# Kernel optimization log

Measured on AMD Instinct MI355X. Metric: run time of the kernel, lower is better.

Reference implementation:

```python
import jax, jax.numpy as jnp
import numpy as np

N = 50000      # nodes
E = 800000     # edges (before self-loops)
H = 4          # heads
C = 32         # hidden per head (hidden*heads = 128); out_channels = 32
IN = 128
NEG_SLOPE = 0.2


def setup_inputs() -> dict:
    key = jax.random.key(0)
    ks = jax.random.split(key, 16)
    s = 0.1
    d = {
        "x": jax.random.normal(ks[0], (N, IN), jnp.float32),
        "edge_index": jax.random.randint(ks[1], (2, E), 0, N),
        "edge_type": jax.random.randint(ks[2], (E,), 0, 38),
        "node_type": jax.random.randint(ks[3], (N,), 0, 4),
        # layer 1: in=128 -> H*C, concat
        "W1": jax.random.normal(ks[4], (IN, H * C), jnp.float32) * s,
        "a1s": jax.random.normal(ks[5], (H, C), jnp.float32) * s,
        "a1d": jax.random.normal(ks[6], (H, C), jnp.float32) * s,
        "b1": jnp.zeros((H * C,), jnp.float32),
        # layer 2: H*C -> H*C, concat
        "W2": jax.random.normal(ks[7], (H * C, H * C), jnp.float32) * s,
        "a2s": jax.random.normal(ks[8], (H, C), jnp.float32) * s,
        "a2d": jax.random.normal(ks[9], (H, C), jnp.float32) * s,
        "b2": jnp.zeros((H * C,), jnp.float32),
        # layer 3: H*C -> C, heads=1, mean (concat=False)
        "W3": jax.random.normal(ks[10], (H * C, C), jnp.float32) * s,
        "a3s": jax.random.normal(ks[11], (1, C), jnp.float32) * s,
        "a3d": jax.random.normal(ks[12], (1, C), jnp.float32) * s,
        "b3": jnp.zeros((C,), jnp.float32),
    }
    return d


def gat_layer(x, src, dst, W, a_s, a_d, b, heads, concat):
    # PyG GATConv (eval mode): linear, per-edge attention logits, segment
    # softmax over incoming edges at dst, weighted scatter-sum, bias.
    h = (x @ W).reshape(N, heads, -1)            # [N, H, C]
    al_s = jnp.einsum('nhc,hc->nh', h, a_s)       # [N, H]
    al_d = jnp.einsum('nhc,hc->nh', h, a_d)
    e = jax.nn.leaky_relu(al_s[src] + al_d[dst], NEG_SLOPE)   # [E', H]
    m = jax.ops.segment_max(e, dst, num_segments=N)            # [N, H]
    p = jnp.exp(e - m[dst])
    z = jax.ops.segment_sum(p, dst, num_segments=N)            # [N, H]
    alpha = p / (z[dst] + 1e-16)                               # [E', H]
    out = jax.ops.segment_sum(h[src] * alpha[..., None], dst, num_segments=N)  # [N, H, C]
    out = out.reshape(N, -1) if concat else out.mean(axis=1)
    return out + b


def reference(x, edge_index, edge_type, node_type,
              W1, a1s, a1d, b1, W2, a2s, a2d, b2, W3, a3s, a3d, b3):
    # add self-loops (PyG GATConv default add_self_loops=True)
    loop = jnp.arange(N, dtype=edge_index.dtype)
    src = jnp.concatenate([edge_index[0], loop])
    dst = jnp.concatenate([edge_index[1], loop])
    h = gat_layer(x, src, dst, W1, a1s, a1d, b1, H, True)
    h = jax.nn.elu(h)
    h = gat_layer(h, src, dst, W2, a2s, a2d, b2, H, True)
    h = jax.nn.elu(h)
    out = gat_layer(h, src, dst, W3, a3s, a3d, b3, 1, False)
    return out
```

## Files before the change

### kernel.cpp

```cpp
#include <hip/hip_runtime.h>
#include <hip/hip_fp16.h>

#define LRELU_SLOPE 0.2f
#define BSH 8
#define EPB 3584

typedef _Float16 f16x8 __attribute__((ext_vector_type(8)));
typedef float f32x4 __attribute__((ext_vector_type(4)));

__device__ __forceinline__ float lrelu(float x) { return x >= 0.0f ? x : LRELU_SLOPE * x; }

__device__ __forceinline__ float sel4(float a, float b, float c, float d, int h) {
  float r = a;
  r = (h == 1) ? b : r;
  r = (h == 2) ? c : r;
  r = (h == 3) ? d : r;
  return r;
}


__device__ __forceinline__ void prep_one(const float* __restrict__ W, __half* __restrict__ out,
                                         int NT, int t) {
  int l = t & 63, f = t >> 6;
  int kt = f / NT, nt = f % NT;
  int k0 = kt * 32 + (l >> 4) * 8;
  int col = nt * 16 + (l & 15);
  union { __half h[8]; float4 v; } u;
#pragma unroll
  for (int j = 0; j < 8; ++j) u.h[j] = (__half)W[(size_t)(k0 + j) * (NT * 16) + col];
  *(float4*)(out + (size_t)t * 8) = u.v;
}


__global__ void k_zero(int* __restrict__ bcnt) { bcnt[threadIdx.x] = 0; }

__global__ __launch_bounds__(256) void k_bcnt(
    const int* __restrict__ dst, int E, int* __restrict__ bcnt, int cntBlocks,
    const float* __restrict__ W1, __half* __restrict__ wf1,
    const float* __restrict__ W2, __half* __restrict__ wf2,
    const float* __restrict__ W3, __half* __restrict__ wf3) {
  if (blockIdx.x >= cntBlocks) {
    int t = (blockIdx.x - cntBlocks) * 256 + threadIdx.x;
    if (t < 2048) prep_one(W1, wf1, 8, t);
    else if (t < 4096) prep_one(W2, wf2, 8, t - 2048);
    else if (t < 4608) prep_one(W3, wf3, 2, t - 4096);
    return;
  }
  __shared__ int c[256];
  int t = threadIdx.x;
  c[t] = 0;
  __syncthreads();
  int e = (blockIdx.x * 256 + t) * 4;
  if (e + 3 < E) {
    int4 d = *(const int4*)&dst[e];
    atomicAdd(&c[d.x >> BSH], 1);
    atomicAdd(&c[d.y >> BSH], 1);
    atomicAdd(&c[d.z >> BSH], 1);
    atomicAdd(&c[d.w >> BSH], 1);
  } else {
    for (; e < E; ++e) atomicAdd(&c[dst[e] >> BSH], 1);
  }
  __syncthreads();
  if (c[t] > 0) atomicAdd(&bcnt[t], c[t]);
}

__global__ __launch_bounds__(256) void k_bscan(const int* __restrict__ bcnt,
                                               int* __restrict__ gcur,
                                               int* __restrict__ bbase, int E) {
  __shared__ int sm[256];
  int t = threadIdx.x;
  int v = bcnt[t];
  sm[t] = v;
  __syncthreads();
#pragma unroll
  for (int off = 1; off < 256; off <<= 1) {
    int u = (t >= off) ? sm[t - off] : 0;
    __syncthreads();
    sm[t] += u;
    __syncthreads();
  }
  int ex = sm[t] - v;
  gcur[t] = ex;
  bbase[t] = ex;
  if (t == 255) bbase[256] = E;
}


__device__ __forceinline__ f16x8 load_a(const float* xp) {
  float4 lo = *(const float4*)xp;
  float4 hi = *(const float4*)(xp + 4);
  f16x8 a;
  a[0] = (_Float16)lo.x; a[1] = (_Float16)lo.y; a[2] = (_Float16)lo.z; a[3] = (_Float16)lo.w;
  a[4] = (_Float16)hi.x; a[5] = (_Float16)hi.y; a[6] = (_Float16)hi.z; a[7] = (_Float16)hi.w;
  return a;
}

__device__ __forceinline__ f16x8 load_a(const __half* xp) {
  return *(const f16x8*)xp;
}

template <int NT, int NH, typename IN, typename OUT>
__device__ __forceinline__ void gemm_body(
    const IN* __restrict__ x, const __half* __restrict__ wfrag,
    const float* __restrict__ a_s, const float* __restrict__ a_d,
    OUT* __restrict__ h, float* __restrict__ als, float* __restrict__ ald,
    int n, int ntiles, int tile, int lane) {
  const f16x8* wf = (const f16x8*)wfrag;
  f16x8 B[4][NT];
#pragma unroll
  for (int kt = 0; kt < 4; ++kt)
#pragma unroll
    for (int nt = 0; nt < NT; ++nt) B[kt][nt] = wf[(kt * NT + nt) * 64 + lane];
  if (tile >= ntiles) return;
  int r0 = tile * 16;
  int arow = r0 + (lane & 15);
  const IN* xp = x + (size_t)arow * 128 + (lane >> 4) * 8;
  bool full = (r0 + 16 <= n);
  f16x8 A[4];
#pragma unroll
  for (int kt = 0; kt < 4; ++kt) {
    if (full || arow < n) A[kt] = load_a(xp + kt * 32);
    else A[kt] = (f16x8){};
  }
  f32x4 acc[NT];
#pragma unroll
  for (int nt = 0; nt < NT; ++nt) acc[nt] = (f32x4){0.f, 0.f, 0.f, 0.f};
#pragma unroll
  for (int kt = 0; kt < 4; ++kt)
#pragma unroll
    for (int nt = 0; nt < NT; ++nt)
      acc[nt] = __builtin_amdgcn_mfma_f32_16x16x32_f16(A[kt], B[kt][nt], acc[nt], 0, 0, 0);
  int cb = lane & 15, rb = (lane >> 4) * 4;
  float asv[NT], adv[NT];
#pragma unroll
  for (int nt = 0; nt < NT; ++nt) {
    asv[nt] = a_s[nt * 16 + cb];
    adv[nt] = a_d[nt * 16 + cb];
  }
#pragma unroll
  for (int r = 0; r < 4; ++r) {
    int row = r0 + rb + r;
    if (!full && row >= n) break;
#pragma unroll
    for (int nt = 0; nt < NT; ++nt)
      h[(size_t)row * (NT * 16) + nt * 16 + cb] = (OUT)acc[nt][r];
    if (NH == 4) {
      float ps[4], pd[4];
#pragma unroll
      for (int hh = 0; hh < 4; ++hh) {
        ps[hh] = acc[2 * hh][r] * asv[2 * hh] + acc[2 * hh + 1][r] * asv[2 * hh + 1];
        pd[hh] = acc[2 * hh][r] * adv[2 * hh] + acc[2 * hh + 1][r] * adv[2 * hh + 1];
      }
#pragma unroll
      for (int off = 1; off < 16; off <<= 1) {
#pragma unroll
        for (int hh = 0; hh < 4; ++hh) {
          ps[hh] += __shfl_xor(ps[hh], off);
          pd[hh] += __shfl_xor(pd[hh], off);
        }
      }
      if (cb < 4) {
        als[row * 4 + cb] = sel4(ps[0], ps[1], ps[2], ps[3], cb);
        ald[row * 4 + cb] = sel4(pd[0], pd[1], pd[2], pd[3], cb);
      }
    } else {
      float ps = acc[0][r] * asv[0] + acc[1][r] * asv[1];
      float pd = acc[0][r] * adv[0] + acc[1][r] * adv[1];
#pragma unroll
      for (int off = 1; off < 16; off <<= 1) {
        ps += __shfl_xor(ps, off);
        pd += __shfl_xor(pd, off);
      }
      if (cb == 0) { als[row] = ps; ald[row] = pd; }
    }
  }
}

template <int NT, int NH, typename IN, typename OUT>
__global__ __launch_bounds__(256, 2) void gemm_mfma(
    const IN* __restrict__ x, const __half* __restrict__ wfrag,
    const float* __restrict__ a_s, const float* __restrict__ a_d,
    OUT* __restrict__ h, float* __restrict__ als, float* __restrict__ ald,
    int n, int ntiles) {
  int lane = threadIdx.x & 63, w = threadIdx.x >> 6;
  gemm_body<NT, NH, IN, OUT>(x, wfrag, a_s, a_d, h, als, ald, n, ntiles,
                             blockIdx.x * 4 + w, lane);
}


__global__ __launch_bounds__(256) void k_bucket_gemm(
    const int* __restrict__ ei, int E, int* __restrict__ gcur, int2* __restrict__ ebuck,
    int bblocks,
    const float* __restrict__ x, const __half* __restrict__ wf1,
    const float* __restrict__ a1s, const float* __restrict__ a1d,
    __half* __restrict__ hA, float* __restrict__ als, float* __restrict__ ald,
    int n, int ntiles) {
  __shared__ int2 stage[EPB];
  __shared__ int cnt[256], offs[256], gbase[256], curl[256], sm[256];
  if (blockIdx.x >= bblocks) {
    int lane = threadIdx.x & 63, w = threadIdx.x >> 6;
    gemm_body<8, 4, float, __half>(x, wf1, a1s, a1d, hA, als, ald, n, ntiles,
                                   (blockIdx.x - bblocks) * 4 + w, lane);
    return;
  }
  int t = threadIdx.x;
  int base = blockIdx.x * EPB;
  int count = E - base;
  if (count > EPB) count = EPB;
  if (count < 0) count = 0;
  cnt[t] = 0;
  __syncthreads();
  for (int i = t; i < count; i += 256) {
    int d = ei[E + base + i];
    atomicAdd(&cnt[d >> BSH], 1);
  }
  __syncthreads();
  sm[t] = cnt[t];
  __syncthreads();
#pragma unroll
  for (int off = 1; off < 256; off <<= 1) {
    int u = (t >= off) ? sm[t - off] : 0;
    __syncthreads();
    sm[t] += u;
    __syncthreads();
  }
  offs[t] = sm[t] - cnt[t];
  curl[t] = sm[t] - cnt[t];
  if (cnt[t] > 0) gbase[t] = atomicAdd(&gcur[t], cnt[t]);
  __syncthreads();
  for (int i = t; i < count; i += 256) {
    int s = ei[base + i];
    int d = ei[E + base + i];
    int r = atomicAdd(&curl[d >> BSH], 1);
    stage[r] = make_int2(s, d);
  }
  __syncthreads();
  for (int i = t; i < count; i += 256) {
    int2 e = stage[i];
    int b = e.y >> BSH;
    ebuck[gbase[b] + (i - offs[b])] = e;
  }
}

__global__ __launch_bounds__(256) void k_fine(const int2* __restrict__ ebuck,
                                              const int* __restrict__ bbase,
                                              int* __restrict__ rowptr,
                                              int* __restrict__ colx, int n, int E) {
  __shared__ int cnt[256], cur[256], sm[256];
  int b = blockIdx.x, t = threadIdx.x;
  int lo = b << BSH;
  int hi = lo + 256;
  if (hi > n) hi = n;
  int nn = hi - lo;
  int ebeg = bbase[b], eend = bbase[b + 1];
  cnt[t] = 0;
  __syncthreads();
  for (int i = ebeg + t; i < eend; i += 256)
    atomicAdd(&cnt[ebuck[i].y - lo], 1);
  __syncthreads();
  sm[t] = cnt[t];
  __syncthreads();
#pragma unroll
  for (int off = 1; off < 256; off <<= 1) {
    int u = (t >= off) ? sm[t - off] : 0;
    __syncthreads();
    sm[t] += u;
    __syncthreads();
  }
  int nodebase = ebeg + sm[t] - cnt[t];
  if (t < nn) {
    rowptr[lo + t] = nodebase;
    cur[t] = nodebase;
  }
  if (t == 0 && b == gridDim.x - 1) rowptr[n] = E;
  __syncthreads();
  for (int i = ebeg + t; i < eend; i += 256) {
    int2 e = ebuck[i];
    int p = atomicAdd(&cur[e.y - lo], 1);
    colx[p] = e.x;
  }
}


__global__ __launch_bounds__(256) void k_agg128(
    const __half* __restrict__ h, const float* __restrict__ als,
    const float* __restrict__ ald, const int* __restrict__ rowptr,
    const int* __restrict__ colx, const float* __restrict__ bias,
    __half* __restrict__ out, int n) {
  int w = threadIdx.x >> 6, lane = threadIdx.x & 63;
  int node = blockIdx.x * 4 + w;
  if (node >= n) return;
  int g = lane >> 4, q = lane & 15, head = q >> 2;
  int beg = rowptr[node], end = rowptr[node + 1];
  float adh = ald[node * 4 + head];
  float acc[8] = {};
  float z = 0.f;
  if (g == 0) {
    float ws = __expf(lrelu(als[node * 4 + head] + adh));
    z = ws;
    float4 raw = *(const float4*)(h + (size_t)node * 128 + q * 8);
    const __half2* hh = (const __half2*)&raw;
#pragma unroll
    for (int j = 0; j < 4; ++j) {
      float2 f = __half22float2(hh[j]);
      acc[2 * j] = ws * f.x;
      acc[2 * j + 1] = ws * f.y;
    }
  }
  for (int e = beg + g; e < end; e += 4) {
    int s = colx[e];
    float wv = __expf(lrelu(als[s * 4 + head] + adh));
    float4 raw = *(const float4*)(h + (size_t)s * 128 + q * 8);
    const __half2* hh = (const __half2*)&raw;
    z += wv;
#pragma unroll
    for (int j = 0; j < 4; ++j) {
      float2 f = __half22float2(hh[j]);
      acc[2 * j] = fmaf(wv, f.x, acc[2 * j]);
      acc[2 * j + 1] = fmaf(wv, f.y, acc[2 * j + 1]);
    }
  }
#pragma unroll
  for (int off = 16; off <= 32; off <<= 1) {
    z += __shfl_xor(z, off);
#pragma unroll
    for (int j = 0; j < 8; ++j) acc[j] += __shfl_xor(acc[j], off);
  }
  if (g == 0) {
    float inv = 1.f / z;
    int c0 = q * 8;
    union { __half h8[8]; float4 v; } u;
#pragma unroll
    for (int j = 0; j < 8; ++j) {
      float v = acc[j] * inv + bias[c0 + j];
      v = (v > 0.f) ? v : (__expf(v) - 1.f);
      u.h8[j] = (__half)v;
    }
    *(float4*)&out[(size_t)node * 128 + c0] = u.v;
  }
}


__global__ __launch_bounds__(256) void k_agg32(
    const __half* __restrict__ h, const float* __restrict__ als,
    const float* __restrict__ ald, const int* __restrict__ rowptr,
    const int* __restrict__ colx, const float* __restrict__ bias,
    float* __restrict__ out, int n) {
  int w = threadIdx.x >> 6, lane = threadIdx.x & 63;
  int node = blockIdx.x * 4 + w;
  if (node >= n) return;
  int g = lane >> 4, q = lane & 15;
  int beg = rowptr[node], end = rowptr[node + 1];
  float ad = ald[node];
  float acc0 = 0.f, acc1 = 0.f, z = 0.f;
  if (g == 0) {
    float ws = __expf(lrelu(als[node] + ad));
    float2 f = __half22float2(*(const __half2*)&h[(size_t)node * 32 + 2 * q]);
    z = ws;
    acc0 = ws * f.x;
    acc1 = ws * f.y;
  }
  for (int e = beg + g; e < end; e += 4) {
    int s = colx[e];
    float wv = __expf(lrelu(als[s] + ad));
    float2 f = __half22float2(*(const __half2*)&h[(size_t)s * 32 + 2 * q]);
    z += wv;
    acc0 = fmaf(wv, f.x, acc0);
    acc1 = fmaf(wv, f.y, acc1);
  }
#pragma unroll
  for (int off = 16; off <= 32; off <<= 1) {
    z += __shfl_xor(z, off);
    acc0 += __shfl_xor(acc0, off);
    acc1 += __shfl_xor(acc1, off);
  }
  if (g == 0) {
    float inv = 1.f / z;
    *(float2*)&out[(size_t)node * 32 + 2 * q] =
        make_float2(acc0 * inv + bias[2 * q], acc1 * inv + bias[2 * q + 1]);
  }
}


extern "C" void kernel_launch(void* const* d_in, const int* in_sizes, int n_in,
                              void* d_out, int out_size, void* d_ws, size_t ws_size,
                              hipStream_t stream) {
  const float* x   = (const float*)d_in[0];
  const int*   ei  = (const int*)d_in[1];
  const float* W1  = (const float*)d_in[4];
  const float* a1s = (const float*)d_in[5];
  const float* a1d = (const float*)d_in[6];
  const float* b1  = (const float*)d_in[7];
  const float* W2  = (const float*)d_in[8];
  const float* a2s = (const float*)d_in[9];
  const float* a2d = (const float*)d_in[10];
  const float* b2  = (const float*)d_in[11];
  const float* W3  = (const float*)d_in[12];
  const float* a3s = (const float*)d_in[13];
  const float* a3d = (const float*)d_in[14];
  const float* b3  = (const float*)d_in[15];
  const int N = in_sizes[0] / 128;
  const int E = in_sizes[1] / 2;
  const int ntiles = (N + 15) / 16;
  const int nbuck = (N + 255) >> BSH;

  char* ws = (char*)d_ws;
  size_t off = 0;
  auto alloc = [&](size_t bytes) -> void* {
    void* p = ws + off;
    off += (bytes + 255) & ~(size_t)255;
    return p;
  };
  __half* hA    = (__half*)alloc((size_t)N * 128 * 2);
  __half* hB    = (__half*)alloc((size_t)N * 128 * 2);
  __half* h32   = (__half*)alloc((size_t)N * 32 * 2);
  float*  als_a = (float*)alloc((size_t)N * 4 * 4);
  float*  ald_a = (float*)alloc((size_t)N * 4 * 4);
  float*  als_b = (float*)alloc((size_t)N * 4 * 4);
  float*  ald_b = (float*)alloc((size_t)N * 4 * 4);
  float*  als1  = (float*)alloc((size_t)N * 4);
  float*  ald1  = (float*)alloc((size_t)N * 4);
  int* rowptr   = (int*)alloc((size_t)(N + 1) * 4);
  int* bcnt     = (int*)alloc(256 * 4);
  int* gcur     = (int*)alloc(256 * 4);
  int* bbase    = (int*)alloc(257 * 4);
  int2* ebuck   = (int2*)alloc((size_t)E * 8);
  int* colx     = (int*)alloc((size_t)E * 4);
  __half* wf1   = (__half*)alloc(4 * 8 * 64 * 8 * 2);
  __half* wf2   = (__half*)alloc(4 * 8 * 64 * 8 * 2);
  __half* wf3   = (__half*)alloc(4 * 2 * 64 * 8 * 2);
  (void)ws_size; (void)n_in; (void)out_size;

  k_zero<<<1, 256, 0, stream>>>(bcnt);
  int cntBlocks = (E / 4 + 255) / 256;
  k_bcnt<<<cntBlocks + 18, 256, 0, stream>>>(ei + E, E, bcnt, cntBlocks,
                                             W1, wf1, W2, wf2, W3, wf3);
  k_bscan<<<1, 256, 0, stream>>>(bcnt, gcur, bbase, E);

  int gblk = (ntiles + 3) / 4;
  int bblocks = (E + EPB - 1) / EPB;
  k_bucket_gemm<<<bblocks + gblk, 256, 0, stream>>>(ei, E, gcur, ebuck, bblocks,
                                                    x, wf1, a1s, a1d, hA, als_a, ald_a,
                                                    N, ntiles);
  k_fine<<<nbuck, 256, 0, stream>>>(ebuck, bbase, rowptr, colx, N, E);

  k_agg128<<<(N + 3) / 4, 256, 0, stream>>>(hA, als_a, ald_a, rowptr, colx, b1, hB, N);
  gemm_mfma<8, 4, __half, __half><<<gblk, 256, 0, stream>>>(hB, wf2, a2s, a2d, hA,
                                                            als_b, ald_b, N, ntiles);
  k_agg128<<<(N + 3) / 4, 256, 0, stream>>>(hA, als_b, ald_b, rowptr, colx, b2, hB, N);
  gemm_mfma<2, 1, __half, __half><<<gblk, 256, 0, stream>>>(hB, wf3, a3s, a3d, h32,
                                                            als1, ald1, N, ntiles);
  k_agg32<<<(N + 3) / 4, 256, 0, stream>>>(h32, als1, ald1, rowptr, colx, b3,
                                           (float*)d_out, N);
}
```

Baseline: 190.0 us.

## Pack bucketed edges into 32-bit words, drop zero kernel, widen aggregation lanes

Bucket counting now writes per-block partial histograms that the scan kernel sums, which removes the zero-init launch and the global atomics. Bucketed edges are packed as (src<<8 | dst&255) in 32 bits, with bucket ids staged separately in shared memory, halving the ebuck traffic. The aggregation kernels now use 8 edge groups of 8 lanes, each lane handling 16 (or 4) channels, which doubles edge-level parallelism and makes per-lane loads wider but adds an extra shuffle-reduction step and more registers per lane. Packing assumes source indices fit in 24 bits.

```diff
diff --git a/kernel.cpp b/kernel.cpp
--- a/kernel.cpp
+++ b/kernel.cpp
@@ -4,6 +4,7 @@
 #define LRELU_SLOPE 0.2f
 #define BSH 8
 #define EPB 3584
+#define EPC 8192
 
 typedef _Float16 f16x8 __attribute__((ext_vector_type(8)));
 typedef float f32x4 __attribute__((ext_vector_type(4)));
@@ -32,10 +33,8 @@
 }
 
 
-__global__ void k_zero(int* __restrict__ bcnt) { bcnt[threadIdx.x] = 0; }
-
 __global__ __launch_bounds__(256) void k_bcnt(
-    const int* __restrict__ dst, int E, int* __restrict__ bcnt, int cntBlocks,
+    const int* __restrict__ dst, int E, int* __restrict__ part, int cntBlocks,
     const float* __restrict__ W1, __half* __restrict__ wf1,
     const float* __restrict__ W2, __half* __restrict__ wf2,
     const float* __restrict__ W3, __half* __restrict__ wf3) {
@@ -50,26 +49,31 @@
   int t = threadIdx.x;
   c[t] = 0;
   __syncthreads();
-  int e = (blockIdx.x * 256 + t) * 4;
-  if (e + 3 < E) {
-    int4 d = *(const int4*)&dst[e];
-    atomicAdd(&c[d.x >> BSH], 1);
-    atomicAdd(&c[d.y >> BSH], 1);
-    atomicAdd(&c[d.z >> BSH], 1);
-    atomicAdd(&c[d.w >> BSH], 1);
-  } else {
-    for (; e < E; ++e) atomicAdd(&c[dst[e] >> BSH], 1);
-  }
-  __syncthreads();
-  if (c[t] > 0) atomicAdd(&bcnt[t], c[t]);
-}
-
-__global__ __launch_bounds__(256) void k_bscan(const int* __restrict__ bcnt,
+  int base = blockIdx.x * EPC;
+#pragma unroll
+  for (int k = 0; k < 8; ++k) {
+    int e = base + (k * 256 + t) * 4;
+    if (e + 3 < E) {
+      int4 d = *(const int4*)&dst[e];
+      atomicAdd(&c[d.x >> BSH], 1);
+      atomicAdd(&c[d.y >> BSH], 1);
+      atomicAdd(&c[d.z >> BSH], 1);
+      atomicAdd(&c[d.w >> BSH], 1);
+    } else {
+      for (int j = e; j < E && j < e + 4; ++j) atomicAdd(&c[dst[j] >> BSH], 1);
+    }
+  }
+  __syncthreads();
+  part[blockIdx.x * 256 + t] = c[t];
+}
+
+__global__ __launch_bounds__(256) void k_bscan(const int* __restrict__ part, int nb,
                                                int* __restrict__ gcur,
                                                int* __restrict__ bbase, int E) {
   __shared__ int sm[256];
   int t = threadIdx.x;
-  int v = bcnt[t];
+  int v = 0;
+  for (int b = 0; b < nb; ++b) v += part[b * 256 + t];
   sm[t] = v;
   __syncthreads();
 #pragma unroll
@@ -189,13 +193,14 @@
 
 
 __global__ __launch_bounds__(256) void k_bucket_gemm(
-    const int* __restrict__ ei, int E, int* __restrict__ gcur, int2* __restrict__ ebuck,
+    const int* __restrict__ ei, int E, int* __restrict__ gcur, int* __restrict__ ebuck,
     int bblocks,
     const float* __restrict__ x, const __half* __restrict__ wf1,
     const float* __restrict__ a1s, const float* __restrict__ a1d,
     __half* __restrict__ hA, float* __restrict__ als, float* __restrict__ ald,
     int n, int ntiles) {
-  __shared__ int2 stage[EPB];
+  __shared__ int stage[EPB];
+  __shared__ unsigned char bucket8[EPB];
   __shared__ int cnt[256], offs[256], gbase[256], curl[256], sm[256];
   if (blockIdx.x >= bblocks) {
     int lane = threadIdx.x & 63, w = threadIdx.x >> 6;
@@ -231,18 +236,19 @@
   for (int i = t; i < count; i += 256) {
     int s = ei[base + i];
     int d = ei[E + base + i];
-    int r = atomicAdd(&curl[d >> BSH], 1);
-    stage[r] = make_int2(s, d);
+    int b = d >> BSH;
+    int r = atomicAdd(&curl[b], 1);
+    stage[r] = (s << 8) | (d & 255);
+    bucket8[r] = (unsigned char)b;
   }
   __syncthreads();
   for (int i = t; i < count; i += 256) {
-    int2 e = stage[i];
-    int b = e.y >> BSH;
-    ebuck[gbase[b] + (i - offs[b])] = e;
-  }
-}
-
-__global__ __launch_bounds__(256) void k_fine(const int2* __restrict__ ebuck,
+    int b = bucket8[i];
+    ebuck[gbase[b] + (i - offs[b])] = stage[i];
+  }
+}
+
+__global__ __launch_bounds__(256) void k_fine(const int* __restrict__ ebuck,
                                               const int* __restrict__ bbase,
                                               int* __restrict__ rowptr,
                                               int* __restrict__ colx, int n, int E) {
@@ -256,7 +262,7 @@
   cnt[t] = 0;
   __syncthreads();
   for (int i = ebeg + t; i < eend; i += 256)
-    atomicAdd(&cnt[ebuck[i].y - lo], 1);
+    atomicAdd(&cnt[ebuck[i] & 255], 1);
   __syncthreads();
   sm[t] = cnt[t];
   __syncthreads();
@@ -275,9 +281,9 @@
   if (t == 0 && b == gridDim.x - 1) rowptr[n] = E;
   __syncthreads();
   for (int i = ebeg + t; i < eend; i += 256) {
-    int2 e = ebuck[i];
-    int p = atomicAdd(&cur[e.y - lo], 1);
-    colx[p] = e.x;
+    int p = ebuck[i];
+    int pos = atomicAdd(&cur[p & 255], 1);
+    colx[pos] = p >> 8;
   }
 }
 
@@ -290,53 +296,67 @@
   int w = threadIdx.x >> 6, lane = threadIdx.x & 63;
   int node = blockIdx.x * 4 + w;
   if (node >= n) return;
-  int g = lane >> 4, q = lane & 15, head = q >> 2;
+  int g = lane >> 3, q = lane & 7, head = q >> 1;
   int beg = rowptr[node], end = rowptr[node + 1];
   float adh = ald[node * 4 + head];
-  float acc[8] = {};
+  float acc[16] = {};
   float z = 0.f;
+  int c0 = q * 16;
   if (g == 0) {
     float ws = __expf(lrelu(als[node * 4 + head] + adh));
     z = ws;
-    float4 raw = *(const float4*)(h + (size_t)node * 128 + q * 8);
-    const __half2* hh = (const __half2*)&raw;
+    float4 ra = *(const float4*)(h + (size_t)node * 128 + c0);
+    float4 rb = *(const float4*)(h + (size_t)node * 128 + c0 + 8);
+    const __half2* ha = (const __half2*)&ra;
+    const __half2* hb = (const __half2*)&rb;
 #pragma unroll
     for (int j = 0; j < 4; ++j) {
-      float2 f = __half22float2(hh[j]);
-      acc[2 * j] = ws * f.x;
-      acc[2 * j + 1] = ws * f.y;
-    }
-  }
-  for (int e = beg + g; e < end; e += 4) {
+      float2 fa = __half22float2(ha[j]);
+      float2 fb = __half22float2(hb[j]);
+      acc[2 * j] = ws * fa.x;
+      acc[2 * j + 1] = ws * fa.y;
+      acc[8 + 2 * j] = ws * fb.x;
+      acc[8 + 2 * j + 1] = ws * fb.y;
+    }
+  }
+  for (int e = beg + g; e < end; e += 8) {
     int s = colx[e];
     float wv = __expf(lrelu(als[s * 4 + head] + adh));
-    float4 raw = *(const float4*)(h + (size_t)s * 128 + q * 8);
-    const __half2* hh = (const __half2*)&raw;
+    float4 ra = *(const float4*)(h + (size_t)s * 128 + c0);
+    float4 rb = *(const float4*)(h + (size_t)s * 128 + c0 + 8);
+    const __half2* ha = (const __half2*)&ra;
+    const __half2* hb = (const __half2*)&rb;
     z += wv;
 #pragma unroll
     for (int j = 0; j < 4; ++j) {
-      float2 f = __half22float2(hh[j]);
-      acc[2 * j] = fmaf(wv, f.x, acc[2 * j]);
-      acc[2 * j + 1] = fmaf(wv, f.y, acc[2 * j + 1]);
-    }
-  }
-#pragma unroll
-  for (int off = 16; off <= 32; off <<= 1) {
+      float2 fa = __half22float2(ha[j]);
+      float2 fb = __half22float2(hb[j]);
+      acc[2 * j] = fmaf(wv, fa.x, acc[2 * j]);
+      acc[2 * j + 1] = fmaf(wv, fa.y, acc[2 * j + 1]);
+      acc[8 + 2 * j] = fmaf(wv, fb.x, acc[8 + 2 * j]);
+      acc[8 + 2 * j + 1] = fmaf(wv, fb.y, acc[8 + 2 * j + 1]);
+    }
+  }
+#pragma unroll
+  for (int off = 8; off <= 32; off <<= 1) {
     z += __shfl_xor(z, off);
 #pragma unroll
-    for (int j = 0; j < 8; ++j) acc[j] += __shfl_xor(acc[j], off);
+    for (int j = 0; j < 16; ++j) acc[j] += __shfl_xor(acc[j], off);
   }
   if (g == 0) {
     float inv = 1.f / z;
-    int c0 = q * 8;
-    union { __half h8[8]; float4 v; } u;
+    union { __half h8[8]; float4 v; } ua, ub;
 #pragma unroll
     for (int j = 0; j < 8; ++j) {
-      float v = acc[j] * inv + bias[c0 + j];
-      v = (v > 0.f) ? v : (__expf(v) - 1.f);
-      u.h8[j] = (__half)v;
-    }
-    *(float4*)&out[(size_t)node * 128 + c0] = u.v;
+      float va = acc[j] * inv + bias[c0 + j];
+      va = (va > 0.f) ? va : (__expf(va) - 1.f);
+      ua.h8[j] = (__half)va;
+      float vb = acc[8 + j] * inv + bias[c0 + 8 + j];
+      vb = (vb > 0.f) ? vb : (__expf(vb) - 1.f);
+      ub.h8[j] = (__half)vb;
+    }
+    *(float4*)&out[(size_t)node * 128 + c0] = ua.v;
+    *(float4*)&out[(size_t)node * 128 + c0 + 8] = ub.v;
   }
 }
 
@@ -349,35 +369,51 @@
   int w = threadIdx.x >> 6, lane = threadIdx.x & 63;
   int node = blockIdx.x * 4 + w;
   if (node >= n) return;
-  int g = lane >> 4, q = lane & 15;
+  int g = lane >> 3, q = lane & 7;
   int beg = rowptr[node], end = rowptr[node + 1];
   float ad = ald[node];
-  float acc0 = 0.f, acc1 = 0.f, z = 0.f;
+  float acc[4] = {};
+  float z = 0.f;
+  int c0 = q * 4;
   if (g == 0) {
     float ws = __expf(lrelu(als[node] + ad));
-    float2 f = __half22float2(*(const __half2*)&h[(size_t)node * 32 + 2 * q]);
+    float2 raw = *(const float2*)(h + (size_t)node * 32 + c0);
+    const __half2* hh = (const __half2*)&raw;
     z = ws;
-    acc0 = ws * f.x;
-    acc1 = ws * f.y;
-  }
-  for (int e = beg + g; e < end; e += 4) {
+#pragma unroll
+    for (int j = 0; j < 2; ++j) {
+      float2 f = __half22float2(hh[j]);
+      acc[2 * j] = ws * f.x;
+      acc[2 * j + 1] = ws * f.y;
+    }
+  }
+  for (int e = beg + g; e < end; e += 8) {
     int s = colx[e];
     float wv = __expf(lrelu(als[s] + ad));
-    float2 f = __half22float2(*(const __half2*)&h[(size_t)s * 32 + 2 * q]);
+    float2 raw = *(const float2*)(h + (size_t)s * 32 + c0);
+    const __half2* hh = (const __half2*)&raw;
     z += wv;
-    acc0 = fmaf(wv, f.x, acc0);
-    acc1 = fmaf(wv, f.y, acc1);
-  }
-#pragma unroll
-  for (int off = 16; off <= 32; off <<= 1) {
+#pragma unroll
+    for (int j = 0; j < 2; ++j) {
+      float2 f = __half22float2(hh[j]);
+      acc[2 * j] = fmaf(wv, f.x, acc[2 * j]);
+      acc[2 * j + 1] = fmaf(wv, f.y, acc[2 * j + 1]);
+    }
+  }
+#pragma unroll
+  for (int off = 8; off <= 32; off <<= 1) {
     z += __shfl_xor(z, off);
-    acc0 += __shfl_xor(acc0, off);
-    acc1 += __shfl_xor(acc1, off);
+#pragma unroll
+    for (int j = 0; j < 4; ++j) acc[j] += __shfl_xor(acc[j], off);
   }
   if (g == 0) {
     float inv = 1.f / z;
-    *(float2*)&out[(size_t)node * 32 + 2 * q] =
-        make_float2(acc0 * inv + bias[2 * q], acc1 * inv + bias[2 * q + 1]);
+    float4 o;
+    o.x = acc[0] * inv + bias[c0];
+    o.y = acc[1] * inv + bias[c0 + 1];
+    o.z = acc[2] * inv + bias[c0 + 2];
+    o.w = acc[3] * inv + bias[c0 + 3];
+    *(float4*)&out[(size_t)node * 32 + c0] = o;
   }
 }
 
@@ -421,21 +457,20 @@
   float*  als1  = (float*)alloc((size_t)N * 4);
   float*  ald1  = (float*)alloc((size_t)N * 4);
   int* rowptr   = (int*)alloc((size_t)(N + 1) * 4);
-  int* bcnt     = (int*)alloc(256 * 4);
   int* gcur     = (int*)alloc(256 * 4);
   int* bbase    = (int*)alloc(257 * 4);
-  int2* ebuck   = (int2*)alloc((size_t)E * 8);
+  int* ebuck    = (int*)alloc((size_t)E * 4);
   int* colx     = (int*)alloc((size_t)E * 4);
   __half* wf1   = (__half*)alloc(4 * 8 * 64 * 8 * 2);
   __half* wf2   = (__half*)alloc(4 * 8 * 64 * 8 * 2);
   __half* wf3   = (__half*)alloc(4 * 2 * 64 * 8 * 2);
+  int cntBlocks = (E + EPC - 1) / EPC;
+  int* part     = (int*)alloc((size_t)cntBlocks * 256 * 4);
   (void)ws_size; (void)n_in; (void)out_size;
 
-  k_zero<<<1, 256, 0, stream>>>(bcnt);
-  int cntBlocks = (E / 4 + 255) / 256;
-  k_bcnt<<<cntBlocks + 18, 256, 0, stream>>>(ei + E, E, bcnt, cntBlocks,
+  k_bcnt<<<cntBlocks + 18, 256, 0, stream>>>(ei + E, E, part, cntBlocks,
                                              W1, wf1, W2, wf2, W3, wf3);
-  k_bscan<<<1, 256, 0, stream>>>(bcnt, gcur, bbase, E);
+  k_bscan<<<1, 256, 0, stream>>>(part, cntBlocks, gcur, bbase, E);
 
   int gblk = (ntiles + 3) / 4;
   int bblocks = (E + EPB - 1) / EPB;
```

Result: faster. 178.0 us (-6.3%).
